# Optimization experiments

Measured on AMD Instinct MI355X. Metric: run time of the kernel, lower is better.

Reference implementation:

```python
import jax, jax.numpy as jnp
import numpy as np

B, T, C = 2, 2048, 2048
NH = 16            # query heads
NKV = NH // 2      # kv heads (GQA)
HD = C // NH       # head dim = 128
N_REP = NH // NKV  # 2


def setup_inputs() -> dict:
    key = jax.random.key(0)
    k1, k2, k3 = jax.random.split(key, 3)
    x = jax.random.normal(k1, (B, T, C), jnp.float32)
    w_attn = jax.random.normal(k2, (C, (NH + 2 * NKV) * HD), jnp.float32) * 0.02
    w_proj = jax.random.normal(k3, (C, C), jnp.float32) * 0.02
    t = jnp.arange(T, dtype=jnp.float32)
    inv_freq = 1.0 / (10000.0 ** (jnp.arange(0, HD, 2, dtype=jnp.float32) / HD))
    freqs = t[:, None] * inv_freq[None, :]  # [T, HD//2]
    return {"x": x, "w_attn": w_attn, "w_proj": w_proj,
            "freqs_cos": jnp.cos(freqs), "freqs_sin": jnp.sin(freqs)}


def _rope(v, cos, sin):
    # v: [B, T, H, HD]; complex multiply on (even, odd) pairs
    vr = v.reshape(*v.shape[:-1], HD // 2, 2)
    x0, x1 = vr[..., 0], vr[..., 1]
    c = cos[None, :, None, :]
    s = sin[None, :, None, :]
    o0 = x0 * c - x1 * s
    o1 = x0 * s + x1 * c
    return jnp.stack([o0, o1], axis=-1).reshape(v.shape)


def reference(x, w_attn, w_proj, freqs_cos, freqs_sin):
    qkv = x @ w_attn  # [B, T, (NH+2*NKV)*HD]
    q, k, v = jnp.split(qkv, [NH * HD, (NH + NKV) * HD], axis=-1)
    q = q.reshape(B, T, NH, HD)
    k = k.reshape(B, T, NKV, HD)
    v = v.reshape(B, T, NKV, HD)
    q = _rope(q, freqs_cos, freqs_sin)
    k = _rope(k, freqs_cos, freqs_sin)
    # GQA: group query heads over kv heads instead of repeating k/v
    q = q.transpose(0, 2, 1, 3).reshape(B, NKV, N_REP, T, HD)  # [B, G, R, T, HD]
    k = k.transpose(0, 2, 1, 3)  # [B, G, T, HD]
    v = v.transpose(0, 2, 1, 3)  # [B, G, T, HD]
    scale = jnp.float32(1.0 / np.sqrt(HD))
    scores = jnp.einsum('bgrqd,bgkd->bgrqk', q, k) * scale
    causal = jnp.tril(jnp.ones((T, T), dtype=bool))
    scores = jnp.where(causal, scores, jnp.float32(-1e30))
    p = jax.nn.softmax(scores, axis=-1)
    y = jnp.einsum('bgrqk,bgkd->bgrqd', p, v)  # [B, G, R, T, HD]
    y = y.reshape(B, NH, T, HD).transpose(0, 2, 1, 3).reshape(B, T, C)
    return y @ w_proj
```

## Files before the change

### kernel.cpp

```cpp
#include <hip/hip_runtime.h>
#include <hip/hip_bf16.h>
#include <stdint.h>
#include <stddef.h>

typedef unsigned short u16;
using bf16x8 = __attribute__((ext_vector_type(8))) short;
using f32x4  = __attribute__((ext_vector_type(4))) float;
using f32x16 = __attribute__((ext_vector_type(16))) float;

#define DEVFN static __device__ __forceinline__

DEVFN u16 f2b(float f){ __hip_bfloat16 h = __float2bfloat16(f); return *reinterpret_cast<u16*>(&h); }
DEVFN float b2f(u16 u){ __hip_bfloat16 h; *reinterpret_cast<u16*>(&h) = u; return __bfloat162float(h); }
DEVFN uint32_t pk2(float a, float b){
  uint32_t r; asm("v_cvt_pk_bf16_f32 %0, %1, %2" : "=v"(r) : "v"(a), "v"(b)); return r;
}
DEVFN float ex2(float x){ float r; asm("v_exp_f32 %0, %1" : "=v"(r) : "v"(x)); return r; }

DEVFN void gload_lds16(const void* g, void* l){
  __builtin_amdgcn_global_load_lds(
      (const __attribute__((address_space(1))) void*)g,
      (__attribute__((address_space(3))) void*)l, 16, 0, 0);
}

__global__ void detect_k(const uint32_t* __restrict__ fc_raw, uint32_t* __restrict__ flag){
  if (threadIdx.x == 0 && blockIdx.x == 0)
    flag[0] = (fc_raw[0] == 0x3F800000u) ? 1u : 0u;
}

__global__ __launch_bounds__(256) void cvtf2_k(const void* __restrict__ inc, const void* __restrict__ ins,
                                               float* __restrict__ outc, float* __restrict__ outs,
                                               int n, const uint32_t* __restrict__ flag){
  const int i = blockIdx.x*256 + threadIdx.x;
  const bool f32in = flag[0] != 0;
  if (i < n){
    outc[i] = f32in ? ((const float*)inc)[i] : b2f(((const u16*)inc)[i]);
  } else if (i < 2*n){
    const int k = i - n;
    outs[k] = f32in ? ((const float*)ins)[k] : b2f(((const u16*)ins)[k]);
  }
}

__global__ __launch_bounds__(256) void cvtx_k(const void* __restrict__ in, u16* __restrict__ out,
                                              int n8, const uint32_t* __restrict__ flag){
  const int i = blockIdx.x*256 + threadIdx.x;
  if (i >= n8) return;
  __align__(16) u16 e[8];
  if (flag[0]){
    const float* f = (const float*)in + (size_t)i*8;
    float4 a = *(const float4*)f, b = *(const float4*)(f+4);
    e[0]=f2b(a.x); e[1]=f2b(a.y); e[2]=f2b(a.z); e[3]=f2b(a.w);
    e[4]=f2b(b.x); e[5]=f2b(b.y); e[6]=f2b(b.z); e[7]=f2b(b.w);
  } else {
    *(uint4*)e = *((const uint4*)in + i);
  }
  *(uint4*)(out + (size_t)i*8) = *(const uint4*)e;
}

__global__ __launch_bounds__(512) void wtrans_k(const void* __restrict__ in, u16* __restrict__ out,
                                                int C, int R, const uint32_t* __restrict__ flag){
  __shared__ __align__(16) u16 tile[64][72];
  const int r0 = blockIdx.y*64, c0 = blockIdx.x*64;
  const int t = threadIdx.x, r = t>>3, cs = (t&7)*8;
  __align__(16) u16 e[8];
  if (flag[0]){
    const float* f = (const float*)in + (size_t)(r0+r)*C + c0 + cs;
    float4 a = *(const float4*)f, b = *(const float4*)(f+4);
    e[0]=f2b(a.x); e[1]=f2b(a.y); e[2]=f2b(a.z); e[3]=f2b(a.w);
    e[4]=f2b(b.x); e[5]=f2b(b.y); e[6]=f2b(b.z); e[7]=f2b(b.w);
  } else {
    *(uint4*)e = *(const uint4*)((const u16*)in + (size_t)(r0+r)*C + c0 + cs);
  }
#pragma unroll
  for (int j=0;j<8;j++) tile[cs+j][r] = e[j];
  __syncthreads();
  uint4 o = *(const uint4*)&tile[r][cs];
  *(uint4*)(out + (size_t)(c0+r)*R + r0 + cs) = o;
}

__global__ __launch_bounds__(512) void vtrans_k(const u16* __restrict__ qkv, u16* __restrict__ vT){
  __shared__ __align__(16) u16 tile[64][72];
  const int z = blockIdx.z, b = z>>3, g = z&7;
  const u16* in = qkv + (size_t)(b*2048)*4096 + 3072 + g*128;
  u16* out = vT + (size_t)z*128*2048;
  const int r0 = blockIdx.y*64, c0 = blockIdx.x*64;
  const int t = threadIdx.x, r = t>>3, cs = (t&7)*8;
  uint4 v = *(const uint4*)(in + (size_t)(r0+r)*4096 + c0 + cs);
  const u16* e = (const u16*)&v;
#pragma unroll
  for (int j=0;j<8;j++) tile[cs+j][r] = e[j];
  __syncthreads();
  uint4 o = *(const uint4*)&tile[r][cs];
  *(uint4*)(out + (size_t)(c0+r)*2048 + r0 + cs) = o;
}

__global__ __launch_bounds__(192) void rope8_k(u16* qkv, const float* __restrict__ fc,
                                               const float* __restrict__ fs){
  const int row = blockIdx.x;
  const int j = threadIdx.x;
  const int p0 = j*8;
  const int t = row & 2047;
  const int i0 = p0 & 63;
  uint4* ptr = (uint4*)(qkv + (size_t)row*4096 + p0*2);
  uint4 u0 = ptr[0], u1 = ptr[1];
  const float* fcp = fc + t*64 + i0;
  const float* fsp = fs + t*64 + i0;
  float4 c0 = *(const float4*)fcp, c1 = *(const float4*)(fcp+4);
  float4 s0 = *(const float4*)fsp, s1 = *(const float4*)(fsp+4);
  const float S2 = (p0 < 1024) ? (0.08838834764831845f * 1.4426950408889634f) : 1.0f;
  uint32_t wd[8] = {u0.x,u0.y,u0.z,u0.w,u1.x,u1.y,u1.z,u1.w};
  const float cc[8] = {c0.x,c0.y,c0.z,c0.w,c1.x,c1.y,c1.z,c1.w};
  const float ss[8] = {s0.x,s0.y,s0.z,s0.w,s1.x,s1.y,s1.z,s1.w};
#pragma unroll
  for (int k=0;k<8;k++){
    const float x0 = b2f((u16)(wd[k] & 0xffff));
    const float x1 = b2f((u16)(wd[k] >> 16));
    const float o0 = (x0*cc[k] - x1*ss[k]) * S2;
    const float o1 = (x0*ss[k] + x1*cc[k]) * S2;
    wd[k] = pk2(o0, o1);
  }
  u0 = make_uint4(wd[0],wd[1],wd[2],wd[3]);
  u1 = make_uint4(wd[4],wd[5],wd[6],wd[7]);
  ptr[0] = u0; ptr[1] = u1;
}

__global__ __launch_bounds__(512) void gemm_p(const u16* __restrict__ A, const u16* __restrict__ Bt,
                                              void* __restrict__ Cv, int M, int N, int K,
                                              const uint32_t* __restrict__ flag, int fin){
  __shared__ __align__(16) u16 L[3*12288];
  const int nwg_x = N>>7;
  int wg = blockIdx.x;
  { const int cpx = (int)gridDim.x >> 3; wg = (wg&7)*cpx + (wg>>3); }
  const int tm = (wg / nwg_x)*256, tn = (wg % nwg_x)*128;
  const int tid = threadIdx.x, w = tid>>6, l = tid&63, lr = l&15, lg = l>>4;
  const int wm = w>>1, wn = w&1;

  f32x4 acc[4][4] = {};

  auto stage = [&](int kt, int buf){
    const int kk = kt*32;
    u16* Lb = &L[buf*12288];
#pragma unroll
    for (int j=0;j<2;j++){
      const int s = j*512 + tid;
      const int row = s>>2, c = s&3;
      const int gch = c ^ ((row ^ (row>>2)) & 3);
      gload_lds16(A + (size_t)(tm + row)*K + kk + gch*8, &Lb[(j*512 + w*64)*8]);
    }
    {
      const int s = tid;
      const int row = s>>2, c = s&3;
      const int gch = c ^ ((row ^ (row>>2)) & 3);
      gload_lds16(Bt + (size_t)(tn + row)*K + kk + gch*8, &Lb[8192 + (w*64)*8]);
    }
  };

  const int nk = K>>5;
  stage(0,0); stage(1,1);
  asm volatile("s_waitcnt vmcnt(3)" ::: "memory");
  __builtin_amdgcn_s_barrier();
  __builtin_amdgcn_sched_barrier(0);

  for (int kt=0; kt<nk; ++kt){
    const int buf = kt % 3;
    if (kt+2 < nk) stage(kt+2, (kt+2) % 3);
    const u16* Ab = &L[buf*12288];
    const u16* Bb = Ab + 8192;
    bf16x8 a[4], b[4];
#pragma unroll
    for (int mi=0;mi<4;mi++){
      const int row = wm*64 + mi*16 + lr;
      a[mi] = *(const bf16x8*)&Ab[row*32 + ((lg ^ ((row ^ (row>>2))&3))*8)];
    }
#pragma unroll
    for (int ni=0;ni<4;ni++){
      const int row = wn*64 + ni*16 + lr;
      b[ni] = *(const bf16x8*)&Bb[row*32 + ((lg ^ ((row ^ (row>>2))&3))*8)];
    }
#pragma unroll
    for (int mi=0;mi<4;mi++)
#pragma unroll
      for (int ni=0;ni<4;ni++)
        acc[mi][ni] = __builtin_amdgcn_mfma_f32_16x16x32_bf16(a[mi], b[ni], acc[mi][ni], 0,0,0);
    __builtin_amdgcn_sched_barrier(0);
    if (kt+2 < nk) asm volatile("s_waitcnt vmcnt(3)" ::: "memory");
    else           asm volatile("s_waitcnt vmcnt(0)" ::: "memory");
    __builtin_amdgcn_s_barrier();
    __builtin_amdgcn_sched_barrier(0);
  }

  const bool of32 = fin && (flag[0] != 0);
#pragma unroll
  for (int mi=0;mi<4;mi++)
#pragma unroll
    for (int ni=0;ni<4;ni++)
#pragma unroll
      for (int reg=0;reg<4;reg++){
        const int row = tm + wm*64 + mi*16 + lg*4 + reg;
        const int col = tn + wn*64 + ni*16 + lr;
        const size_t idx = (size_t)row*N + col;
        const float v = acc[mi][ni][reg];
        if (of32) ((float*)Cv)[idx] = v;
        else      ((u16*)Cv)[idx]   = f2b(v);
      }
}

__global__ __launch_bounds__(512) void gemm_p2(const u16* __restrict__ A, const u16* __restrict__ Bt,
                                               void* __restrict__ Cv, int M, int N, int K,
                                               const uint32_t* __restrict__ flag, int fin){
  __shared__ __align__(16) u16 L[3*16384];
  const int nwg_x = N>>8;
  int wg = blockIdx.x;
  { const int cpx = (int)gridDim.x >> 3; wg = (wg&7)*cpx + (wg>>3); }
  const int tm = (wg / nwg_x)*256, tn = (wg % nwg_x)*256;
  const int tid = threadIdx.x, w = tid>>6, l = tid&63, lr = l&15, lg = l>>4;
  const int wm = w>>2, wn = w&3;

  f32x4 acc[8][4] = {};

  auto stage = [&](int kt, int buf){
    const int kk = kt*32;
    u16* Lb = &L[buf*16384];
#pragma unroll
    for (int j=0;j<2;j++){
      const int s = j*512 + tid;
      const int row = s>>2, c = s&3;
      const int gch = c ^ ((row ^ (row>>2)) & 3);
      gload_lds16(A + (size_t)(tm + row)*K + kk + gch*8, &Lb[(j*512 + w*64)*8]);
    }
#pragma unroll
    for (int j=0;j<2;j++){
      const int s = j*512 + tid;
      const int row = s>>2, c = s&3;
      const int gch = c ^ ((row ^ (row>>2)) & 3);
      gload_lds16(Bt + (size_t)(tn + row)*K + kk + gch*8, &Lb[8192 + (j*512 + w*64)*8]);
    }
  };

  const int nk = K>>5;
  stage(0,0); stage(1,1);
  asm volatile("s_waitcnt vmcnt(4)" ::: "memory");
  __builtin_amdgcn_s_barrier();
  __builtin_amdgcn_sched_barrier(0);

  for (int kt=0; kt<nk; ++kt){
    const int buf = kt % 3;
    if (kt+2 < nk) stage(kt+2, (kt+2) % 3);
    const u16* Ab = &L[buf*16384];
    const u16* Bb = Ab + 8192;
    bf16x8 a[8], b[4];
#pragma unroll
    for (int mi=0;mi<8;mi++){
      const int row = wm*128 + mi*16 + lr;
      a[mi] = *(const bf16x8*)&Ab[row*32 + ((lg ^ ((row ^ (row>>2))&3))*8)];
    }
#pragma unroll
    for (int ni=0;ni<4;ni++){
      const int row = wn*64 + ni*16 + lr;
      b[ni] = *(const bf16x8*)&Bb[row*32 + ((lg ^ ((row ^ (row>>2))&3))*8)];
    }
#pragma unroll
    for (int mi=0;mi<8;mi++)
#pragma unroll
      for (int ni=0;ni<4;ni++)
        acc[mi][ni] = __builtin_amdgcn_mfma_f32_16x16x32_bf16(a[mi], b[ni], acc[mi][ni], 0,0,0);
    __builtin_amdgcn_sched_barrier(0);
    if (kt+2 < nk) asm volatile("s_waitcnt vmcnt(4)" ::: "memory");
    else           asm volatile("s_waitcnt vmcnt(0)" ::: "memory");
    __builtin_amdgcn_s_barrier();
    __builtin_amdgcn_sched_barrier(0);
  }

  const bool of32 = fin && (flag[0] != 0);
#pragma unroll
  for (int mi=0;mi<8;mi++)
#pragma unroll
    for (int ni=0;ni<4;ni++)
#pragma unroll
      for (int reg=0;reg<4;reg++){
        const int row = tm + wm*128 + mi*16 + lg*4 + reg;
        const int col = tn + wn*64 + ni*16 + lr;
        const size_t idx = (size_t)row*N + col;
        const float v = acc[mi][ni][reg];
        if (of32) ((float*)Cv)[idx] = v;
        else      ((u16*)Cv)[idx]   = f2b(v);
      }
}

__global__ __launch_bounds__(512, 1) void attn_k(const u16* __restrict__ qkv,
                                                 const u16* __restrict__ vT,
                                                 u16* __restrict__ y){
  __shared__ __align__(16) u16 KV[2][2][16384];
  const int i0 = blockIdx.x;
  const int g  = i0 & 7;
  const int r1 = i0 >> 3;
  const int hl = r1 & 1;
  const int vq = (r1 >> 1) & 7;
  const int b  = r1 >> 4;
  const int h  = g*2 + hl;

  const int tid = threadIdx.x;
  const int w = tid >> 6, l = tid & 63;
  const int grp = w >> 2, wq = w & 3;
  const int lq = l & 31;
  const int hi = l >> 5;

  const u16* kg = qkv + (size_t)(b*2048)*4096 + 2048 + g*128;
  const u16* vg = vT  + (size_t)(b*8+g)*128*2048;

  const int rk = tid >> 2, cb = tid & 3;
  uint4 kpre[4], vpre[4];
  auto loadT = [&](int kvbase){
#pragma unroll
    for (int j=0;j<4;j++){
      const int ch = cb + j*4;
      kpre[j] = *(const uint4*)(kg + (size_t)(kvbase + rk)*4096 + ch*8);
      vpre[j] = *(const uint4*)(vg + (size_t)rk*2048 + kvbase + ch*8);
    }
  };
  auto writeT = [&](int buf){
    u16* Kd = &KV[buf][rk>>6][0];
    const int rl = rk & 63;
#pragma unroll
    for (int j=0;j<4;j++){
      const int ch = cb + j*4;
      *(uint4*)&Kd[rl*128 + ((ch ^ (rl&15))*8)] = kpre[j];
    }
#pragma unroll
    for (int j=0;j<4;j++){
      const int ch = cb + j*4;
      u16* Vd = &KV[buf][ch>>3][8192];
      *(uint4*)&Vd[rk*64 + (((ch&7) ^ (rk&7))*8)] = vpre[j];
    }
  };

  int qt = vq;
  const int nA = vq + 1;
  bf16x8 qf[8];
  f32x16 yacc[4];
  float mrow, lsum;

  auto loadQ = [&]{
    const size_t qrow = (size_t)(b*2048 + qt*128 + wq*32 + lq);
    const u16* qp = qkv + qrow*4096 + h*128 + hi*8;
#pragma unroll
    for (int ds=0; ds<8; ++ds) qf[ds] = *(const bf16x8*)(qp + ds*16);
  };
  auto resetAcc = [&]{
#pragma unroll
    for (int dt=0; dt<4; ++dt)
#pragma unroll
      for (int r=0; r<16; ++r) yacc[dt][r] = 0.f;
    mrow = -1e30f; lsum = 0.f;
  };

  auto mergePhase = [&](u16* Mb){
    float* Mm = (float*)Mb; float* Ml = Mm + 128;
    u16* MOs = Mb + 512 + wq*4096;
    __syncthreads();
    if (grp == 1){
      if (l < 32){ Mm[wq*32 + l] = mrow; Ml[wq*32 + l] = lsum; }
#pragma unroll
      for (int dt=0; dt<4; ++dt)
#pragma unroll
        for (int rq=0; rq<4; ++rq){
          const int d0 = dt*32 + rq*8 + hi*4;
          uint32_t lo = pk2(yacc[dt][rq*4+0], yacc[dt][rq*4+1]);
          uint32_t hi2= pk2(yacc[dt][rq*4+2], yacc[dt][rq*4+3]);
          const int idx = (lq*128 + d0) ^ ((lq&7)<<3);
          *(uint2*)&MOs[idx] = make_uint2(lo, hi2);
        }
    }
    __syncthreads();
    if (grp == 0){
      const float mo = Mm[wq*32 + lq], lo_ = Ml[wq*32 + lq];
      const float ms = fmaxf(mrow, mo);
      const float ce = ex2(mrow - ms), co = ex2(mo - ms);
      const float inv = 1.f / (lsum*ce + lo_*co);
#pragma unroll
      for (int dt=0; dt<4; ++dt)
#pragma unroll
        for (int rq=0; rq<4; ++rq){
          const int d0 = dt*32 + rq*8 + hi*4;
          const int idx = (lq*128 + d0) ^ ((lq&7)<<3);
          uint2 pr = *(const uint2*)&MOs[idx];
          const float yo0 = b2f((u16)(pr.x & 0xffff)), yo1 = b2f((u16)(pr.x >> 16));
          const float yo2 = b2f((u16)(pr.y & 0xffff)), yo3 = b2f((u16)(pr.y >> 16));
          uint32_t lo = pk2((yacc[dt][rq*4+0]*ce + yo0*co)*inv, (yacc[dt][rq*4+1]*ce + yo1*co)*inv);
          uint32_t hi2= pk2((yacc[dt][rq*4+2]*ce + yo2*co)*inv, (yacc[dt][rq*4+3]*ce + yo3*co)*inv);
          *(uint2*)&MOs[idx] = make_uint2(lo, hi2);
        }
    }
    __syncthreads();
    const int qb2 = b*2048 + qt*128 + wq*32;
#pragma unroll
    for (int p=0; p<2; ++p){
      const int row = grp*16 + p*8 + (l>>3);
      const int gc = l & 7;
      const int idx0 = (row*128 + gc*16) ^ ((row&7)<<3);
      const int idx1 = (row*128 + gc*16 + 8) ^ ((row&7)<<3);
      uint4 v0 = *(const uint4*)&MOs[idx0];
      uint4 v1 = *(const uint4*)&MOs[idx1];
      u16* yp = y + (size_t)(qb2 + row)*2048 + h*128 + gc*16;
      *(uint4*)yp = v0;
      *(uint4*)(yp + 8) = v1;
    }
    __syncthreads();
  };

  loadT(0); writeT(0); __syncthreads();
  loadQ(); resetAcc();

  for (int s=0; s<17; ++s){
    if (s == nA){
      mergePhase(&KV[(nA&1)^1][0][0]);
      qt = 15 - vq;
      loadQ(); resetAcc();
    }
    const int sj = (s < nA) ? s : s - nA;
    const int kvbase = sj*128;
    if (s+1 < 17){
      const int s2 = s+1;
      const int sj2 = (s2 < nA) ? s2 : s2 - nA;
      loadT(sj2*128);
    }
    const u16* Kb = &KV[s&1][grp][0];
    const u16* Vb = Kb + 8192;
    const int tilebase = kvbase + grp*64;
    const int qmin = qt*128 + wq*32;
    const int qrow = qmin + lq;

    if (tilebase <= qmin + 31){
      f32x16 sc[2];
#pragma unroll
      for (int t=0;t<2;t++)
#pragma unroll
        for (int r=0;r<16;r++) sc[t][r] = 0.f;
      __builtin_amdgcn_s_setprio(1);
#pragma unroll
      for (int t=0; t<2; ++t){
        const int r = t*32 + lq;
        const int rsw = r & 15;
#pragma unroll
        for (int ds=0; ds<8; ++ds){
          const bf16x8 kf = *(const bf16x8*)&Kb[r*128 + (((2*ds+hi) ^ rsw)*8)];
          sc[t] = __builtin_amdgcn_mfma_f32_32x32x16_bf16(kf, qf[ds], sc[t], 0,0,0);
        }
      }
      __builtin_amdgcn_s_setprio(0);

      if (tilebase + 63 > qmin){
#pragma unroll
        for (int t=0;t<2;t++)
#pragma unroll
          for (int r=0;r<16;r++){
            const int kp = tilebase + t*32 + (r&3) + 8*(r>>2) + 4*hi;
            if (kp > qrow) sc[t][r] = -1e30f;
          }
      }

      float mx[16];
#pragma unroll
      for (int r=0;r<16;r++) mx[r] = fmaxf(sc[0][r], sc[1][r]);
#pragma unroll
      for (int off=8; off>0; off>>=1)
#pragma unroll
        for (int r=0;r<8;r++)
          if (r < off) mx[r] = fmaxf(mx[r], mx[r+off]);
      float pmax = fmaxf(mx[0], __shfl_xor(mx[0], 32));

      if (!__all(pmax <= mrow + 8.f)){
        const float mnew = fmaxf(mrow, pmax);
        const float corr = ex2(mrow - mnew);
        mrow = mnew; lsum *= corr;
#pragma unroll
        for (int dt=0;dt<4;dt++)
#pragma unroll
          for (int r=0;r<16;r++) yacc[dt][r] *= corr;
      }

#pragma unroll
      for (int t=0;t<2;t++)
#pragma unroll
        for (int r=0;r<16;r++) sc[t][r] = ex2(sc[t][r] - mrow);
      float sm[16];
#pragma unroll
      for (int r=0;r<16;r++) sm[r] = sc[0][r] + sc[1][r];
#pragma unroll
      for (int off=8; off>0; off>>=1)
#pragma unroll
        for (int r=0;r<8;r++)
          if (r < off) sm[r] += sm[r+off];
      lsum += sm[0] + __shfl_xor(sm[0], 32);

      __align__(16) uint32_t pw[4][4];
#pragma unroll
      for (int t=0;t<2;t++)
#pragma unroll
        for (int half=0; half<2; ++half){
          const int q8 = half*8;
          const uint32_t X0 = pk2(sc[t][q8+0], sc[t][q8+1]);
          const uint32_t X1 = pk2(sc[t][q8+2], sc[t][q8+3]);
          const uint32_t X2 = pk2(sc[t][q8+4], sc[t][q8+5]);
          const uint32_t X3 = pk2(sc[t][q8+6], sc[t][q8+7]);
          const uint32_t pX0 = (uint32_t)__shfl_xor((int)X0, 32);
          const uint32_t pX1 = (uint32_t)__shfl_xor((int)X1, 32);
          const uint32_t pX2 = (uint32_t)__shfl_xor((int)X2, 32);
          const uint32_t pX3 = (uint32_t)__shfl_xor((int)X3, 32);
          const int ks = t*2 + half;
          pw[ks][0] = hi ? pX2 : X0;
          pw[ks][1] = hi ? pX3 : X1;
          pw[ks][2] = hi ? X2 : pX0;
          pw[ks][3] = hi ? X3 : pX1;
        }

      __builtin_amdgcn_s_setprio(1);
#pragma unroll
      for (int dt=0; dt<4; ++dt){
        const int d = dt*32 + lq;
        const int dsw = d & 7;
#pragma unroll
        for (int ks=0; ks<4; ++ks){
          const bf16x8 vf = *(const bf16x8*)&Vb[d*64 + (((2*ks+hi) ^ dsw)*8)];
          yacc[dt] = __builtin_amdgcn_mfma_f32_32x32x16_bf16(vf, *(const bf16x8*)&pw[ks][0], yacc[dt], 0,0,0);
        }
      }
      __builtin_amdgcn_s_setprio(0);
    }

    if (s+1 < 17) writeT((s&1)^1);
    __syncthreads();
  }
  mergePhase(&KV[0][0][0]);
}

extern "C" void kernel_launch(void* const* d_in, const int* in_sizes, int n_in,
                              void* d_out, int out_size, void* d_ws, size_t ws_size,
                              hipStream_t stream){
  char* ws = (char*)d_ws;
  const size_t MB = 1048576;
  uint32_t* flag = (uint32_t*)(ws);
  float* fcF = (float*)(ws + 1*MB);
  float* fsF = (float*)(ws + 1*MB + 524288);
  u16* xb   = (u16*)(ws + 2*MB);
  u16* waT  = (u16*)(ws + 18*MB);
  u16* wpT  = (u16*)(ws + 34*MB);
  u16* qkvb = (u16*)(ws + 42*MB);
  u16* vTb  = (u16*)(ws + 74*MB);
  u16* yb   = xb;

  detect_k<<<1, 64, 0, stream>>>((const uint32_t*)d_in[3], flag);
  cvtf2_k <<<1024, 256, 0, stream>>>(d_in[3], d_in[4], fcF, fsF, 131072, flag);
  cvtx_k  <<<4096, 256, 0, stream>>>(d_in[0], xb, 1048576, flag);
  wtrans_k<<<dim3(64,32,1), 512, 0, stream>>>(d_in[1], waT, 4096, 2048, flag);
  wtrans_k<<<dim3(32,32,1), 512, 0, stream>>>(d_in[2], wpT, 2048, 2048, flag);
  gemm_p2 <<<dim3(256,1,1), 512, 0, stream>>>(xb, waT, qkvb, 4096, 4096, 2048, flag, 0);
  rope8_k <<<dim3(4096,1,1), 192, 0, stream>>>(qkvb, fcF, fsF);
  vtrans_k<<<dim3(2,32,16), 512, 0, stream>>>(qkvb, vTb);
  attn_k  <<<dim3(256,1,1), 512, 0, stream>>>(qkvb, vTb, yb);
  gemm_p  <<<dim3(256,1,1), 512, 0, stream>>>(yb, wpT, d_out, 4096, 2048, 2048, flag, 1);
}
```

Before: 257.1 us.

## Replace both GEMM kernels with a 4-wave 256x256 tile, double-buffered GEMM

Both GEMM kernels are replaced by a single kernel using 4 waves of 256 threads, where each wave computes a 128x128 sub-tile (8x8 MFMA accumulators). The LDS pipeline drops from triple to double buffering. The output projection now runs on 128 workgroups with 256x256 tiles instead of 256 workgroups with 256x128 tiles. The aim is more register-level reuse of A/B fragments per LDS load, at the cost of much higher register pressure, shallower prefetch, and fewer workgroups than CUs for the projection GEMM.

```diff
diff --git a/kernel.cpp b/kernel.cpp
--- a/kernel.cpp
+++ b/kernel.cpp
@@ -124,149 +124,67 @@
   ptr[0] = u0; ptr[1] = u1;
 }
 
-__global__ __launch_bounds__(512) void gemm_p(const u16* __restrict__ A, const u16* __restrict__ Bt,
-                                              void* __restrict__ Cv, int M, int N, int K,
-                                              const uint32_t* __restrict__ flag, int fin){
-  __shared__ __align__(16) u16 L[3*12288];
-  const int nwg_x = N>>7;
-  int wg = blockIdx.x;
-  { const int cpx = (int)gridDim.x >> 3; wg = (wg&7)*cpx + (wg>>3); }
-  const int tm = (wg / nwg_x)*256, tn = (wg % nwg_x)*128;
-  const int tid = threadIdx.x, w = tid>>6, l = tid&63, lr = l&15, lg = l>>4;
-  const int wm = w>>1, wn = w&1;
-
-  f32x4 acc[4][4] = {};
-
-  auto stage = [&](int kt, int buf){
-    const int kk = kt*32;
-    u16* Lb = &L[buf*12288];
-#pragma unroll
-    for (int j=0;j<2;j++){
-      const int s = j*512 + tid;
-      const int row = s>>2, c = s&3;
-      const int gch = c ^ ((row ^ (row>>2)) & 3);
-      gload_lds16(A + (size_t)(tm + row)*K + kk + gch*8, &Lb[(j*512 + w*64)*8]);
-    }
-    {
-      const int s = tid;
-      const int row = s>>2, c = s&3;
-      const int gch = c ^ ((row ^ (row>>2)) & 3);
-      gload_lds16(Bt + (size_t)(tn + row)*K + kk + gch*8, &Lb[8192 + (w*64)*8]);
-    }
-  };
-
-  const int nk = K>>5;
-  stage(0,0); stage(1,1);
-  asm volatile("s_waitcnt vmcnt(3)" ::: "memory");
-  __builtin_amdgcn_s_barrier();
-  __builtin_amdgcn_sched_barrier(0);
-
-  for (int kt=0; kt<nk; ++kt){
-    const int buf = kt % 3;
-    if (kt+2 < nk) stage(kt+2, (kt+2) % 3);
-    const u16* Ab = &L[buf*12288];
-    const u16* Bb = Ab + 8192;
-    bf16x8 a[4], b[4];
-#pragma unroll
-    for (int mi=0;mi<4;mi++){
-      const int row = wm*64 + mi*16 + lr;
-      a[mi] = *(const bf16x8*)&Ab[row*32 + ((lg ^ ((row ^ (row>>2))&3))*8)];
-    }
-#pragma unroll
-    for (int ni=0;ni<4;ni++){
-      const int row = wn*64 + ni*16 + lr;
-      b[ni] = *(const bf16x8*)&Bb[row*32 + ((lg ^ ((row ^ (row>>2))&3))*8)];
-    }
-#pragma unroll
-    for (int mi=0;mi<4;mi++)
-#pragma unroll
-      for (int ni=0;ni<4;ni++)
-        acc[mi][ni] = __builtin_amdgcn_mfma_f32_16x16x32_bf16(a[mi], b[ni], acc[mi][ni], 0,0,0);
-    __builtin_amdgcn_sched_barrier(0);
-    if (kt+2 < nk) asm volatile("s_waitcnt vmcnt(3)" ::: "memory");
-    else           asm volatile("s_waitcnt vmcnt(0)" ::: "memory");
-    __builtin_amdgcn_s_barrier();
-    __builtin_amdgcn_sched_barrier(0);
-  }
-
-  const bool of32 = fin && (flag[0] != 0);
-#pragma unroll
-  for (int mi=0;mi<4;mi++)
-#pragma unroll
-    for (int ni=0;ni<4;ni++)
-#pragma unroll
-      for (int reg=0;reg<4;reg++){
-        const int row = tm + wm*64 + mi*16 + lg*4 + reg;
-        const int col = tn + wn*64 + ni*16 + lr;
-        const size_t idx = (size_t)row*N + col;
-        const float v = acc[mi][ni][reg];
-        if (of32) ((float*)Cv)[idx] = v;
-        else      ((u16*)Cv)[idx]   = f2b(v);
-      }
-}
-
-__global__ __launch_bounds__(512) void gemm_p2(const u16* __restrict__ A, const u16* __restrict__ Bt,
-                                               void* __restrict__ Cv, int M, int N, int K,
-                                               const uint32_t* __restrict__ flag, int fin){
-  __shared__ __align__(16) u16 L[3*16384];
+__global__ __launch_bounds__(256, 1) void gemm_p3(const u16* __restrict__ A, const u16* __restrict__ Bt,
+                                                  void* __restrict__ Cv, int M, int N, int K,
+                                                  const uint32_t* __restrict__ flag, int fin){
+  __shared__ __align__(16) u16 L[2*16384];
   const int nwg_x = N>>8;
   int wg = blockIdx.x;
   { const int cpx = (int)gridDim.x >> 3; wg = (wg&7)*cpx + (wg>>3); }
   const int tm = (wg / nwg_x)*256, tn = (wg % nwg_x)*256;
   const int tid = threadIdx.x, w = tid>>6, l = tid&63, lr = l&15, lg = l>>4;
-  const int wm = w>>2, wn = w&3;
-
-  f32x4 acc[8][4] = {};
+  const int wm = w>>1, wn = w&1;
+
+  f32x4 acc[8][8] = {};
 
   auto stage = [&](int kt, int buf){
     const int kk = kt*32;
     u16* Lb = &L[buf*16384];
 #pragma unroll
-    for (int j=0;j<2;j++){
-      const int s = j*512 + tid;
+    for (int j=0;j<4;j++){
+      const int s = j*256 + tid;
       const int row = s>>2, c = s&3;
       const int gch = c ^ ((row ^ (row>>2)) & 3);
-      gload_lds16(A + (size_t)(tm + row)*K + kk + gch*8, &Lb[(j*512 + w*64)*8]);
-    }
-#pragma unroll
-    for (int j=0;j<2;j++){
-      const int s = j*512 + tid;
+      gload_lds16(A + (size_t)(tm + row)*K + kk + gch*8, &Lb[(j*256 + w*64)*8]);
+    }
+#pragma unroll
+    for (int j=0;j<4;j++){
+      const int s = j*256 + tid;
       const int row = s>>2, c = s&3;
       const int gch = c ^ ((row ^ (row>>2)) & 3);
-      gload_lds16(Bt + (size_t)(tn + row)*K + kk + gch*8, &Lb[8192 + (j*512 + w*64)*8]);
+      gload_lds16(Bt + (size_t)(tn + row)*K + kk + gch*8, &Lb[8192 + (j*256 + w*64)*8]);
     }
   };
 
   const int nk = K>>5;
-  stage(0,0); stage(1,1);
-  asm volatile("s_waitcnt vmcnt(4)" ::: "memory");
+  stage(0,0);
+  asm volatile("s_waitcnt vmcnt(0)" ::: "memory");
   __builtin_amdgcn_s_barrier();
   __builtin_amdgcn_sched_barrier(0);
 
   for (int kt=0; kt<nk; ++kt){
-    const int buf = kt % 3;
-    if (kt+2 < nk) stage(kt+2, (kt+2) % 3);
+    const int buf = kt & 1;
+    if (kt+1 < nk) stage(kt+1, buf^1);
     const u16* Ab = &L[buf*16384];
     const u16* Bb = Ab + 8192;
-    bf16x8 a[8], b[4];
+    bf16x8 a[8], b[8];
 #pragma unroll
     for (int mi=0;mi<8;mi++){
       const int row = wm*128 + mi*16 + lr;
       a[mi] = *(const bf16x8*)&Ab[row*32 + ((lg ^ ((row ^ (row>>2))&3))*8)];
     }
 #pragma unroll
-    for (int ni=0;ni<4;ni++){
-      const int row = wn*64 + ni*16 + lr;
+    for (int ni=0;ni<8;ni++){
+      const int row = wn*128 + ni*16 + lr;
       b[ni] = *(const bf16x8*)&Bb[row*32 + ((lg ^ ((row ^ (row>>2))&3))*8)];
     }
 #pragma unroll
     for (int mi=0;mi<8;mi++)
 #pragma unroll
-      for (int ni=0;ni<4;ni++)
+      for (int ni=0;ni<8;ni++)
         acc[mi][ni] = __builtin_amdgcn_mfma_f32_16x16x32_bf16(a[mi], b[ni], acc[mi][ni], 0,0,0);
     __builtin_amdgcn_sched_barrier(0);
-    if (kt+2 < nk) asm volatile("s_waitcnt vmcnt(4)" ::: "memory");
-    else           asm volatile("s_waitcnt vmcnt(0)" ::: "memory");
+    asm volatile("s_waitcnt vmcnt(0)" ::: "memory");
     __builtin_amdgcn_s_barrier();
     __builtin_amdgcn_sched_barrier(0);
   }
@@ -275,11 +193,11 @@
 #pragma unroll
   for (int mi=0;mi<8;mi++)
 #pragma unroll
-    for (int ni=0;ni<4;ni++)
+    for (int ni=0;ni<8;ni++)
 #pragma unroll
       for (int reg=0;reg<4;reg++){
         const int row = tm + wm*128 + mi*16 + lg*4 + reg;
-        const int col = tn + wn*64 + ni*16 + lr;
+        const int col = tn + wn*128 + ni*16 + lr;
         const size_t idx = (size_t)row*N + col;
         const float v = acc[mi][ni][reg];
         if (of32) ((float*)Cv)[idx] = v;
@@ -554,9 +472,9 @@
   cvtx_k  <<<4096, 256, 0, stream>>>(d_in[0], xb, 1048576, flag);
   wtrans_k<<<dim3(64,32,1), 512, 0, stream>>>(d_in[1], waT, 4096, 2048, flag);
   wtrans_k<<<dim3(32,32,1), 512, 0, stream>>>(d_in[2], wpT, 2048, 2048, flag);
-  gemm_p2 <<<dim3(256,1,1), 512, 0, stream>>>(xb, waT, qkvb, 4096, 4096, 2048, flag, 0);
+  gemm_p3 <<<dim3(256,1,1), 256, 0, stream>>>(xb, waT, qkvb, 4096, 4096, 2048, flag, 0);
   rope8_k <<<dim3(4096,1,1), 192, 0, stream>>>(qkvb, fcF, fsF);
   vtrans_k<<<dim3(2,32,16), 512, 0, stream>>>(qkvb, vTb);
   attn_k  <<<dim3(256,1,1), 512, 0, stream>>>(qkvb, vTb, yb);
-  gemm_p  <<<dim3(256,1,1), 512, 0, stream>>>(yb, wpT, d_out, 4096, 2048, 2048, flag, 1);
-}
+  gemm_p3 <<<dim3(128,1,1), 256, 0, stream>>>(yb, wpT, d_out, 4096, 2048, 2048, flag, 1);
+}
```

After: 300.9 us. +17.0%, slower.

## Fuse RoPE and Q scaling into QKV GEMM epilogue, deepen LDS pipeline

Applied to the files above, without the earlier changes.

Removes the separate rope8_k pass by applying the rotary embedding and the softmax scale inside the QKV GEMM epilogue. Paired even/odd columns are exchanged between adjacent lanes with a shuffle, and cos/sin are read from global memory per element. It also grows the LDS ring from three to four stages with prefetch distance three, and adjusts the vmcnt waits to match. This saves one full read-modify-write of the QKV buffer and one launch. In exchange the epilogue does scattered scalar loads of cos/sin, and the larger LDS footprint may limit occupancy.

```diff
diff --git a/kernel.cpp b/kernel.cpp
--- a/kernel.cpp
+++ b/kernel.cpp
@@ -94,36 +94,6 @@
   *(uint4*)(out + (size_t)(c0+r)*2048 + r0 + cs) = o;
 }
 
-__global__ __launch_bounds__(192) void rope8_k(u16* qkv, const float* __restrict__ fc,
-                                               const float* __restrict__ fs){
-  const int row = blockIdx.x;
-  const int j = threadIdx.x;
-  const int p0 = j*8;
-  const int t = row & 2047;
-  const int i0 = p0 & 63;
-  uint4* ptr = (uint4*)(qkv + (size_t)row*4096 + p0*2);
-  uint4 u0 = ptr[0], u1 = ptr[1];
-  const float* fcp = fc + t*64 + i0;
-  const float* fsp = fs + t*64 + i0;
-  float4 c0 = *(const float4*)fcp, c1 = *(const float4*)(fcp+4);
-  float4 s0 = *(const float4*)fsp, s1 = *(const float4*)(fsp+4);
-  const float S2 = (p0 < 1024) ? (0.08838834764831845f * 1.4426950408889634f) : 1.0f;
-  uint32_t wd[8] = {u0.x,u0.y,u0.z,u0.w,u1.x,u1.y,u1.z,u1.w};
-  const float cc[8] = {c0.x,c0.y,c0.z,c0.w,c1.x,c1.y,c1.z,c1.w};
-  const float ss[8] = {s0.x,s0.y,s0.z,s0.w,s1.x,s1.y,s1.z,s1.w};
-#pragma unroll
-  for (int k=0;k<8;k++){
-    const float x0 = b2f((u16)(wd[k] & 0xffff));
-    const float x1 = b2f((u16)(wd[k] >> 16));
-    const float o0 = (x0*cc[k] - x1*ss[k]) * S2;
-    const float o1 = (x0*ss[k] + x1*cc[k]) * S2;
-    wd[k] = pk2(o0, o1);
-  }
-  u0 = make_uint4(wd[0],wd[1],wd[2],wd[3]);
-  u1 = make_uint4(wd[4],wd[5],wd[6],wd[7]);
-  ptr[0] = u0; ptr[1] = u1;
-}
-
 __global__ __launch_bounds__(512) void gemm_p(const u16* __restrict__ A, const u16* __restrict__ Bt,
                                               void* __restrict__ Cv, int M, int N, int K,
                                               const uint32_t* __restrict__ flag, int fin){
@@ -205,10 +175,10 @@
       }
 }
 
-__global__ __launch_bounds__(512) void gemm_p2(const u16* __restrict__ A, const u16* __restrict__ Bt,
-                                               void* __restrict__ Cv, int M, int N, int K,
-                                               const uint32_t* __restrict__ flag, int fin){
-  __shared__ __align__(16) u16 L[3*16384];
+__global__ __launch_bounds__(512) void gemm_q(const u16* __restrict__ A, const u16* __restrict__ Bt,
+                                              u16* __restrict__ Cv, int M, int N, int K,
+                                              const float* __restrict__ fc, const float* __restrict__ fs){
+  __shared__ __align__(16) u16 L[4*16384];
   const int nwg_x = N>>8;
   int wg = blockIdx.x;
   { const int cpx = (int)gridDim.x >> 3; wg = (wg&7)*cpx + (wg>>3); }
@@ -238,14 +208,14 @@
   };
 
   const int nk = K>>5;
-  stage(0,0); stage(1,1);
-  asm volatile("s_waitcnt vmcnt(4)" ::: "memory");
+  stage(0,0); stage(1,1); stage(2,2);
+  asm volatile("s_waitcnt vmcnt(8)" ::: "memory");
   __builtin_amdgcn_s_barrier();
   __builtin_amdgcn_sched_barrier(0);
 
   for (int kt=0; kt<nk; ++kt){
-    const int buf = kt % 3;
-    if (kt+2 < nk) stage(kt+2, (kt+2) % 3);
+    const int buf = kt & 3;
+    if (kt+3 < nk) stage(kt+3, (kt+3) & 3);
     const u16* Ab = &L[buf*16384];
     const u16* Bb = Ab + 8192;
     bf16x8 a[8], b[4];
@@ -265,26 +235,38 @@
       for (int ni=0;ni<4;ni++)
         acc[mi][ni] = __builtin_amdgcn_mfma_f32_16x16x32_bf16(a[mi], b[ni], acc[mi][ni], 0,0,0);
     __builtin_amdgcn_sched_barrier(0);
-    if (kt+2 < nk) asm volatile("s_waitcnt vmcnt(4)" ::: "memory");
-    else           asm volatile("s_waitcnt vmcnt(0)" ::: "memory");
+    if      (kt+3 < nk) asm volatile("s_waitcnt vmcnt(8)" ::: "memory");
+    else if (kt+2 < nk) asm volatile("s_waitcnt vmcnt(4)" ::: "memory");
+    else                asm volatile("s_waitcnt vmcnt(0)" ::: "memory");
     __builtin_amdgcn_s_barrier();
     __builtin_amdgcn_sched_barrier(0);
   }
 
-  const bool of32 = fin && (flag[0] != 0);
+  const float S2q = 0.08838834764831845f * 1.4426950408889634f;
 #pragma unroll
   for (int mi=0;mi<8;mi++)
 #pragma unroll
-    for (int ni=0;ni<4;ni++)
+    for (int ni=0;ni<4;ni++){
+      const int col = tn + wn*64 + ni*16 + lr;
+      const bool doRope = col < 3072;
+      const float S2 = (col < 2048) ? S2q : 1.0f;
+      const int fi = (col >> 1) & 63;
+      const bool odd = (lr & 1) != 0;
 #pragma unroll
       for (int reg=0;reg<4;reg++){
         const int row = tm + wm*128 + mi*16 + lg*4 + reg;
-        const int col = tn + wn*64 + ni*16 + lr;
-        const size_t idx = (size_t)row*N + col;
-        const float v = acc[mi][ni][reg];
-        if (of32) ((float*)Cv)[idx] = v;
-        else      ((u16*)Cv)[idx]   = f2b(v);
+        float x = acc[mi][ni][reg];
+        const float xp = __shfl_xor(x, 1);
+        if (doRope){
+          const int t = row & 2047;
+          const float c = fc[t*64 + fi];
+          const float s = fs[t*64 + fi];
+          x = odd ? (xp*s + x*c) : (x*c - xp*s);
+          x *= S2;
+        }
+        Cv[(size_t)row*N + col] = f2b(x);
       }
+    }
 }
 
 __global__ __launch_bounds__(512, 1) void attn_k(const u16* __restrict__ qkv,
@@ -554,8 +536,7 @@
   cvtx_k  <<<4096, 256, 0, stream>>>(d_in[0], xb, 1048576, flag);
   wtrans_k<<<dim3(64,32,1), 512, 0, stream>>>(d_in[1], waT, 4096, 2048, flag);
   wtrans_k<<<dim3(32,32,1), 512, 0, stream>>>(d_in[2], wpT, 2048, 2048, flag);
-  gemm_p2 <<<dim3(256,1,1), 512, 0, stream>>>(xb, waT, qkvb, 4096, 4096, 2048, flag, 0);
-  rope8_k <<<dim3(4096,1,1), 192, 0, stream>>>(qkvb, fcF, fsF);
+  gemm_q  <<<dim3(256,1,1), 512, 0, stream>>>(xb, waT, qkvb, 4096, 4096, 2048, fcF, fsF);
   vtrans_k<<<dim3(2,32,16), 512, 0, stream>>>(qkvb, vTb);
   attn_k  <<<dim3(256,1,1), 512, 0, stream>>>(qkvb, vTb, yb);
   gemm_p  <<<dim3(256,1,1), 512, 0, stream>>>(yb, wpT, d_out, 4096, 2048, 2048, flag, 1);
```

After: 265.3 us. +3.2%, slower.
